# Kernel optimization log

Hardware: AMD Instinct MI355X
Metric: run time of the kernel (lower is better)

Reference implementation:

```python
import jax, jax.numpy as jnp
import numpy as np

TOP_K = 2

def setup_inputs() -> dict:
    key = jax.random.key(0)
    k1, k2 = jax.random.split(key)
    T, D, E = 16384, 2048, 64  # num_tokens, d_model, num_experts
    x = jax.random.normal(k1, (T, D), dtype=jnp.float32)
    Wg = jax.random.normal(k2, (D, E), dtype=jnp.float32) / np.sqrt(D)
    return {"x": x, "Wg": Wg}

def reference(x, Wg):
    T, E = x.shape[0], Wg.shape[1]
    # gate logits + softmax over experts
    logits = x @ Wg                                   # [T, E]
    probs = jax.nn.softmax(logits, axis=-1)           # [T, E]
    # top-k expert selection, renormalize selected weights
    top_vals, top_idx = jax.lax.top_k(probs, TOP_K)   # [T, K]
    top_vals = top_vals / jnp.sum(top_vals, axis=-1, keepdims=True)
    # scatter sparse gate weights into dense [T, E]
    rows = jnp.arange(T)[:, None]                     # [T, 1]
    gate_weights = jnp.zeros_like(probs).at[rows, top_idx].set(top_vals)
    # load-balance aux loss: E * sum_e f_e * P_e
    mask = jnp.sum(jax.nn.one_hot(top_idx, E, dtype=probs.dtype), axis=1)  # [T, E]
    f = jnp.mean(mask, axis=0)    # fraction of tokens routed to each expert
    P = jnp.mean(probs, axis=0)   # mean router prob per expert
    aux_loss = E * jnp.sum(f * P)
    return gate_weights, top_idx, aux_loss
```

## Files before the change

### kernel.cpp

```cpp
#include <hip/hip_runtime.h>


typedef __attribute__((ext_vector_type(8))) _Float16 half8;
typedef __attribute__((ext_vector_type(4))) float f32x4;

constexpr int DD  = 2048;
constexpr int EE  = 64;
constexpr int BM  = 16;
constexpr int BK  = 64;
constexpr int NCH = DD / BK;

#define WVM(N) asm volatile("s_waitcnt vmcnt(" #N ")" ::: "memory")
#define BAR()  asm volatile("s_barrier" ::: "memory")

__global__ __launch_bounds__(256) void wsplit_kernel(
    const float* __restrict__ Wg, _Float16* __restrict__ wF)
{
    __shared__ float xl[32][65];
    const int tid = threadIdx.x;
    const int kc  = blockIdx.x;
    const int k0  = kc * 32;
#pragma unroll
    for (int r = 0; r < 2; ++r) {
        int slot = tid + r * 256;
        int row = slot >> 4, c4 = (slot & 15) << 2;
        *(float4*)&xl[row][c4] = *(const float4*)&Wg[(size_t)(k0 + row) * EE + c4];
    }
    __syncthreads();
    const int t = tid >> 6, l = tid & 63;
    const int e  = t * 16 + (l & 15);
    const int kl = (l >> 4) * 8;
    half8 hh, ll;
#pragma unroll
    for (int j = 0; j < 8; ++j) {
        float v = xl[kl + j][e];
        _Float16 h = (_Float16)v;
        hh[j] = h;
        ll[j] = (_Float16)((v - (float)h) * 4096.f);
    }
    const size_t base = ((size_t)(kc * 4 + t) * 2) * 512 + (size_t)l * 8;
    *(half8*)&wF[base]       = hh;
    *(half8*)&wF[base + 512] = ll;
}

__global__ __launch_bounds__(256, 4) void gate_kernel(
    const float* __restrict__ x, const _Float16* __restrict__ wF,
    float* __restrict__ gate_out, float* __restrict__ idx_out,
    float* __restrict__ pSum, float* __restrict__ pCnt)
{
    __shared__ __align__(16) float xs[4][BM][BK];
    __shared__ float red[2][BM][68];
    __shared__ float auxsm[2][4][64];

    const int tid  = threadIdx.x;
    const int wv   = tid >> 6;
    const int lane = tid & 63;
    const int kh   = wv & 1;
    const int nh   = wv >> 1;
    const size_t tok0 = (size_t)blockIdx.x * BM;
    const float* xg = x + tok0 * DD;

    const int srow = tid >> 4;
    const int scb  = (tid & 15) << 4;
    const int ssb  = scb ^ ((srow & 7) << 5);
    auto stageX = [&](int buf, int c) {
        __builtin_amdgcn_global_load_lds(
            xg + (size_t)srow * DD + c * BK + (ssb >> 2),
            &xs[buf][srow][scb >> 2], 16, 0, 0);
    };

    const size_t tile0 = (((size_t)kh * 4 + nh * 2) * 2) * 512 + (size_t)lane * 8;
    const _Float16* w00 = wF + tile0;
    const _Float16* w01 = wF + tile0 + 512;
    const _Float16* w10 = wF + tile0 + 1024;
    const _Float16* w11 = wF + tile0 + 1536;
    half8 wA0, wA1, wA2, wA3, wB0, wB1, wB2, wB3;

#define LOADW(R0, R1, R2, R3, c)                                               \
    do { const size_t o = (size_t)(c) * 8192;                                  \
         R0 = *(const half8*)(w00 + o); R1 = *(const half8*)(w01 + o);         \
         R2 = *(const half8*)(w10 + o); R3 = *(const half8*)(w11 + o); } while (0)

    f32x4 aH0 = {0.f,0.f,0.f,0.f}, aL0 = {0.f,0.f,0.f,0.f};
    f32x4 aH1 = {0.f,0.f,0.f,0.f}, aL1 = {0.f,0.f,0.f,0.f};

    const int rrow = lane & 15;
    const int rfb  = (kh * 128 + (lane >> 4) * 32) ^ ((rrow & 7) << 5);

#define COMPUTE(buf, W0, W1, W2, W3)                                           \
    do {                                                                       \
        const float* p = (const float*)((const char*)&xs[buf][rrow][0] + rfb); \
        float4 xa = *(const float4*)p;                                         \
        float4 xb = *(const float4*)(p + 4);                                   \
        half8 ah, al; float v;                                                 \
        v = xa.x; { _Float16 h=(_Float16)v; ah[0]=h; al[0]=(_Float16)((v-(float)h)*4096.f); } \
        v = xa.y; { _Float16 h=(_Float16)v; ah[1]=h; al[1]=(_Float16)((v-(float)h)*4096.f); } \
        v = xa.z; { _Float16 h=(_Float16)v; ah[2]=h; al[2]=(_Float16)((v-(float)h)*4096.f); } \
        v = xa.w; { _Float16 h=(_Float16)v; ah[3]=h; al[3]=(_Float16)((v-(float)h)*4096.f); } \
        v = xb.x; { _Float16 h=(_Float16)v; ah[4]=h; al[4]=(_Float16)((v-(float)h)*4096.f); } \
        v = xb.y; { _Float16 h=(_Float16)v; ah[5]=h; al[5]=(_Float16)((v-(float)h)*4096.f); } \
        v = xb.z; { _Float16 h=(_Float16)v; ah[6]=h; al[6]=(_Float16)((v-(float)h)*4096.f); } \
        v = xb.w; { _Float16 h=(_Float16)v; ah[7]=h; al[7]=(_Float16)((v-(float)h)*4096.f); } \
        aH0 = __builtin_amdgcn_mfma_f32_16x16x32_f16(ah, W0, aH0, 0, 0, 0);    \
        aL0 = __builtin_amdgcn_mfma_f32_16x16x32_f16(ah, W1, aL0, 0, 0, 0);    \
        aL0 = __builtin_amdgcn_mfma_f32_16x16x32_f16(al, W0, aL0, 0, 0, 0);    \
        aH1 = __builtin_amdgcn_mfma_f32_16x16x32_f16(ah, W2, aH1, 0, 0, 0);    \
        aL1 = __builtin_amdgcn_mfma_f32_16x16x32_f16(ah, W3, aL1, 0, 0, 0);    \
        aL1 = __builtin_amdgcn_mfma_f32_16x16x32_f16(al, W2, aL1, 0, 0, 0);    \
    } while (0)

    stageX(0, 0);
    stageX(1, 1);
    LOADW(wA0, wA1, wA2, wA3, 0);
    stageX(2, 2);
    LOADW(wB0, wB1, wB2, wB3, 1);

#pragma unroll 1
    for (int c = 0; c < NCH; ++c) {
        if (c < NCH - 1) { WVM(5); } else { WVM(0); }
        BAR();
        if (c & 1) {
            COMPUTE(c & 3, wB0, wB1, wB2, wB3);
            if (c + 2 < NCH) LOADW(wB0, wB1, wB2, wB3, c + 2);
        } else {
            COMPUTE(c & 3, wA0, wA1, wA2, wA3);
            if (c + 2 < NCH) LOADW(wA0, wA1, wA2, wA3, c + 2);
        }
        if (c + 3 < NCH) stageX((c + 3) & 3, c + 3);
        BAR();
    }
#undef LOADW
#undef COMPUTE

    const float inv = 1.f / 4096.f;
#pragma unroll
    for (int e = 0; e < 4; ++e) {
        const int row = (lane >> 4) * 4 + e;
        red[kh][row][nh * 32 + (lane & 15)]      = aH0[e] + aL0[e] * inv;
        red[kh][row][nh * 32 + 16 + (lane & 15)] = aH1[e] + aL1[e] * inv;
    }
    __syncthreads();

    float sumP_acc = 0.f;
    float cnt_acc  = 0.f;
#pragma unroll 1
    for (int tt = 0; tt < 4; ++tt) {
        const int tl = wv * 4 + tt;
        const size_t t = tok0 + tl;
        float v = red[0][tl][lane] + red[1][tl][lane];

        float m = v;
#pragma unroll
        for (int off = 32; off; off >>= 1) m = fmaxf(m, __shfl_xor(m, off, 64));
        float p = expf(v - m);
        float s = p;
#pragma unroll
        for (int off = 32; off; off >>= 1) s += __shfl_xor(s, off, 64);
        float prob = p / s;
        sumP_acc += prob;

        float bv = prob; int bi = lane;
#pragma unroll
        for (int off = 32; off; off >>= 1) {
            float ov = __shfl_xor(bv, off, 64);
            int   oi = __shfl_xor(bi, off, 64);
            if (ov > bv || (ov == bv && oi < bi)) { bv = ov; bi = oi; }
        }
        float v2 = (lane == bi) ? -1.f : prob;
        float bv2 = v2; int bi2 = lane;
#pragma unroll
        for (int off = 32; off; off >>= 1) {
            float ov = __shfl_xor(bv2, off, 64);
            int   oi = __shfl_xor(bi2, off, 64);
            if (ov > bv2 || (ov == bv2 && oi < bi2)) { bv2 = ov; bi2 = oi; }
        }

        float denom = bv + bv2;
        float g1 = bv / denom, g2 = bv2 / denom;
        float g = (lane == bi) ? g1 : ((lane == bi2) ? g2 : 0.f);
        gate_out[t * EE + lane] = g;
        if (lane == 0) {
            idx_out[2 * t]     = (float)bi;
            idx_out[2 * t + 1] = (float)bi2;
        }
        cnt_acc += (lane == bi)  ? 1.f : 0.f;
        cnt_acc += (lane == bi2) ? 1.f : 0.f;
    }

    auxsm[0][wv][lane] = sumP_acc;
    auxsm[1][wv][lane] = cnt_acc;
    __syncthreads();
    if (wv == 0) {
        float sp = 0.f, c2 = 0.f;
#pragma unroll
        for (int w = 0; w < 4; ++w) {
            sp += auxsm[0][w][lane];
            c2 += auxsm[1][w][lane];
        }
        pSum[(size_t)blockIdx.x * 64 + lane] = sp;
        pCnt[(size_t)blockIdx.x * 64 + lane] = c2;
    }
}

__global__ __launch_bounds__(1024) void aux_kernel(
    const float* __restrict__ pSum, const float* __restrict__ pCnt,
    float* __restrict__ aux_out, int nblocks, float scale)
{
    const int tid  = threadIdx.x;
    const int wv   = tid >> 6;
    const int lane = tid & 63;
    __shared__ float smem[2][16][64];

    float sp[4] = {0.f, 0.f, 0.f, 0.f};
    float cc[4] = {0.f, 0.f, 0.f, 0.f};
    for (int b = wv * 4; b < nblocks; b += 64) {
#pragma unroll
        for (int u = 0; u < 4; ++u) {
            sp[u] += pSum[(size_t)(b + u) * 64 + lane];
            cc[u] += pCnt[(size_t)(b + u) * 64 + lane];
        }
    }
    smem[0][wv][lane] = (sp[0] + sp[1]) + (sp[2] + sp[3]);
    smem[1][wv][lane] = (cc[0] + cc[1]) + (cc[2] + cc[3]);
    __syncthreads();
    if (wv == 0) {
        float SP = 0.f, C = 0.f;
#pragma unroll
        for (int w = 0; w < 16; ++w) {
            SP += smem[0][w][lane];
            C  += smem[1][w][lane];
        }
        float prod = SP * C;
#pragma unroll
        for (int off = 32; off; off >>= 1) prod += __shfl_xor(prod, off, 64);
        if (lane == 0) aux_out[0] = prod * scale;
    }
}

extern "C" void kernel_launch(void* const* d_in, const int* in_sizes, int n_in,
                              void* d_out, int out_size, void* d_ws, size_t ws_size,
                              hipStream_t stream) {
    const float* x  = (const float*)d_in[0];
    const float* Wg = (const float*)d_in[1];
    const int T = in_sizes[0] / DD;

    float* out      = (float*)d_out;
    float* gate_out = out;
    float* idx_out  = out + (size_t)T * EE;
    float* aux_out  = idx_out + (size_t)T * 2;

    const int nblocks = T / BM;
    _Float16* wF = (_Float16*)d_ws;
    float* pSum = (float*)(wF + (size_t)64 * 4 * 2 * 512);
    float* pCnt = pSum + (size_t)nblocks * 64;

    wsplit_kernel<<<64, 256, 0, stream>>>(Wg, wF);
    gate_kernel<<<nblocks, 256, 0, stream>>>(x, wF, gate_out, idx_out, pSum, pCnt);

    const float scale = (float)EE / ((float)T * (float)T);
    aux_kernel<<<1, 1024, 0, stream>>>(pSum, pCnt, aux_out, nblocks, scale);
}
```

Before: 56.55 us.

## Split K across four waves with full expert width and wider K chunks

Each of the four waves now owns a quarter of a 128-wide K chunk and computes all 64 experts, instead of a 2x2 split over K and experts. The K chunk doubles, the x staging ring drops from four buffers to three, and the epilogue buffers share LDS with the staging buffers through a union. Weight fragments are loaded inside compute instead of being register double-buffered. The aim is fewer loop iterations and barriers with more MFMA work per wave, but weight-load latency is now exposed within each step and there is one less buffer of prefetch depth.

Measured after the change: 53.89 us. 4.7% less time.

```diff
diff --git a/kernel.cpp b/kernel.cpp
--- a/kernel.cpp
+++ b/kernel.cpp
@@ -7,7 +7,7 @@
 constexpr int DD  = 2048;
 constexpr int EE  = 64;
 constexpr int BM  = 16;
-constexpr int BK  = 64;
+constexpr int BK  = 128;
 constexpr int NCH = DD / BK;
 
 #define WVM(N) asm volatile("s_waitcnt vmcnt(" #N ")" ::: "memory")
@@ -38,7 +38,7 @@
         hh[j] = h;
         ll[j] = (_Float16)((v - (float)h) * 4096.f);
     }
-    const size_t base = ((size_t)(kc * 4 + t) * 2) * 512 + (size_t)l * 8;
+    const size_t base = (size_t)(kc * 8 + t * 2) * 512 + (size_t)l * 8;
     *(half8*)&wF[base]       = hh;
     *(half8*)&wF[base + 512] = ll;
 }
@@ -48,96 +48,91 @@
     float* __restrict__ gate_out, float* __restrict__ idx_out,
     float* __restrict__ pSum, float* __restrict__ pCnt)
 {
-    __shared__ __align__(16) float xs[4][BM][BK];
-    __shared__ float red[2][BM][68];
-    __shared__ float auxsm[2][4][64];
+    __shared__ __align__(16) union {
+        float xs[3][BM][BK];
+        struct { float red[4][BM][68]; float auxsm[2][4][64]; } ep;
+    } sm;
 
     const int tid  = threadIdx.x;
-    const int wv   = tid >> 6;
+    const int kq   = tid >> 6;
     const int lane = tid & 63;
-    const int kh   = wv & 1;
-    const int nh   = wv >> 1;
     const size_t tok0 = (size_t)blockIdx.x * BM;
     const float* xg = x + tok0 * DD;
 
-    const int srow = tid >> 4;
-    const int scb  = (tid & 15) << 4;
-    const int ssb  = scb ^ ((srow & 7) << 5);
     auto stageX = [&](int buf, int c) {
-        __builtin_amdgcn_global_load_lds(
-            xg + (size_t)srow * DD + c * BK + (ssb >> 2),
-            &xs[buf][srow][scb >> 2], 16, 0, 0);
+#pragma unroll
+        for (int r = 0; r < 2; ++r) {
+            int slot = tid + r * 256;
+            int row  = slot >> 5;
+            int cb   = (slot & 31) << 4;
+            int sb   = cb ^ ((row & 7) << 5);
+            __builtin_amdgcn_global_load_lds(
+                xg + (size_t)row * DD + c * BK + (sb >> 2),
+                &sm.xs[buf][row][cb >> 2], 16, 0, 0);
+        }
     };
 
-    const size_t tile0 = (((size_t)kh * 4 + nh * 2) * 2) * 512 + (size_t)lane * 8;
-    const _Float16* w00 = wF + tile0;
-    const _Float16* w01 = wF + tile0 + 512;
-    const _Float16* w10 = wF + tile0 + 1024;
-    const _Float16* w11 = wF + tile0 + 1536;
-    half8 wA0, wA1, wA2, wA3, wB0, wB1, wB2, wB3;
-
-#define LOADW(R0, R1, R2, R3, c)                                               \
-    do { const size_t o = (size_t)(c) * 8192;                                  \
-         R0 = *(const half8*)(w00 + o); R1 = *(const half8*)(w01 + o);         \
-         R2 = *(const half8*)(w10 + o); R3 = *(const half8*)(w11 + o); } while (0)
-
-    f32x4 aH0 = {0.f,0.f,0.f,0.f}, aL0 = {0.f,0.f,0.f,0.f};
-    f32x4 aH1 = {0.f,0.f,0.f,0.f}, aL1 = {0.f,0.f,0.f,0.f};
+    f32x4 aH[4], aL[4];
+#pragma unroll
+    for (int t = 0; t < 4; ++t) {
+        aH[t] = (f32x4){0.f, 0.f, 0.f, 0.f};
+        aL[t] = (f32x4){0.f, 0.f, 0.f, 0.f};
+    }
 
     const int rrow = lane & 15;
-    const int rfb  = (kh * 128 + (lane >> 4) * 32) ^ ((rrow & 7) << 5);
-
-#define COMPUTE(buf, W0, W1, W2, W3)                                           \
-    do {                                                                       \
-        const float* p = (const float*)((const char*)&xs[buf][rrow][0] + rfb); \
-        float4 xa = *(const float4*)p;                                         \
-        float4 xb = *(const float4*)(p + 4);                                   \
-        half8 ah, al; float v;                                                 \
-        v = xa.x; { _Float16 h=(_Float16)v; ah[0]=h; al[0]=(_Float16)((v-(float)h)*4096.f); } \
-        v = xa.y; { _Float16 h=(_Float16)v; ah[1]=h; al[1]=(_Float16)((v-(float)h)*4096.f); } \
-        v = xa.z; { _Float16 h=(_Float16)v; ah[2]=h; al[2]=(_Float16)((v-(float)h)*4096.f); } \
-        v = xa.w; { _Float16 h=(_Float16)v; ah[3]=h; al[3]=(_Float16)((v-(float)h)*4096.f); } \
-        v = xb.x; { _Float16 h=(_Float16)v; ah[4]=h; al[4]=(_Float16)((v-(float)h)*4096.f); } \
-        v = xb.y; { _Float16 h=(_Float16)v; ah[5]=h; al[5]=(_Float16)((v-(float)h)*4096.f); } \
-        v = xb.z; { _Float16 h=(_Float16)v; ah[6]=h; al[6]=(_Float16)((v-(float)h)*4096.f); } \
-        v = xb.w; { _Float16 h=(_Float16)v; ah[7]=h; al[7]=(_Float16)((v-(float)h)*4096.f); } \
-        aH0 = __builtin_amdgcn_mfma_f32_16x16x32_f16(ah, W0, aH0, 0, 0, 0);    \
-        aL0 = __builtin_amdgcn_mfma_f32_16x16x32_f16(ah, W1, aL0, 0, 0, 0);    \
-        aL0 = __builtin_amdgcn_mfma_f32_16x16x32_f16(al, W0, aL0, 0, 0, 0);    \
-        aH1 = __builtin_amdgcn_mfma_f32_16x16x32_f16(ah, W2, aH1, 0, 0, 0);    \
-        aL1 = __builtin_amdgcn_mfma_f32_16x16x32_f16(ah, W3, aL1, 0, 0, 0);    \
-        aL1 = __builtin_amdgcn_mfma_f32_16x16x32_f16(al, W2, aL1, 0, 0, 0);    \
-    } while (0)
+    const int rb   = (kq * 128 + ((lane >> 4) * 32)) ^ ((rrow & 7) << 5);
+
+    auto compute = [&](int buf, int c) {
+        const _Float16* wb = wF + (size_t)(c * 4 + kq) * 4096 + (size_t)lane * 8;
+        half8 wh[4], wl[4];
+#pragma unroll
+        for (int t = 0; t < 4; ++t) {
+            wh[t] = *(const half8*)(wb + (t * 2) * 512);
+            wl[t] = *(const half8*)(wb + (t * 2 + 1) * 512);
+        }
+        const float* p = (const float*)((const char*)&sm.xs[buf][rrow][0] + rb);
+        float4 xa = *(const float4*)p;
+        float4 xb = *(const float4*)(p + 4);
+        half8 ah, al;
+        {
+            float v;
+            v = xa.x; { _Float16 h=(_Float16)v; ah[0]=h; al[0]=(_Float16)((v-(float)h)*4096.f); }
+            v = xa.y; { _Float16 h=(_Float16)v; ah[1]=h; al[1]=(_Float16)((v-(float)h)*4096.f); }
+            v = xa.z; { _Float16 h=(_Float16)v; ah[2]=h; al[2]=(_Float16)((v-(float)h)*4096.f); }
+            v = xa.w; { _Float16 h=(_Float16)v; ah[3]=h; al[3]=(_Float16)((v-(float)h)*4096.f); }
+            v = xb.x; { _Float16 h=(_Float16)v; ah[4]=h; al[4]=(_Float16)((v-(float)h)*4096.f); }
+            v = xb.y; { _Float16 h=(_Float16)v; ah[5]=h; al[5]=(_Float16)((v-(float)h)*4096.f); }
+            v = xb.z; { _Float16 h=(_Float16)v; ah[6]=h; al[6]=(_Float16)((v-(float)h)*4096.f); }
+            v = xb.w; { _Float16 h=(_Float16)v; ah[7]=h; al[7]=(_Float16)((v-(float)h)*4096.f); }
+        }
+#pragma unroll
+        for (int t = 0; t < 4; ++t) {
+            aH[t] = __builtin_amdgcn_mfma_f32_16x16x32_f16(ah, wh[t], aH[t], 0, 0, 0);
+            aL[t] = __builtin_amdgcn_mfma_f32_16x16x32_f16(ah, wl[t], aL[t], 0, 0, 0);
+            aL[t] = __builtin_amdgcn_mfma_f32_16x16x32_f16(al, wh[t], aL[t], 0, 0, 0);
+        }
+    };
 
     stageX(0, 0);
     stageX(1, 1);
-    LOADW(wA0, wA1, wA2, wA3, 0);
-    stageX(2, 2);
-    LOADW(wB0, wB1, wB2, wB3, 1);
 
 #pragma unroll 1
     for (int c = 0; c < NCH; ++c) {
-        if (c < NCH - 1) { WVM(5); } else { WVM(0); }
+        if (c < NCH - 1) { WVM(2); } else { WVM(0); }
         BAR();
-        if (c & 1) {
-            COMPUTE(c & 3, wB0, wB1, wB2, wB3);
-            if (c + 2 < NCH) LOADW(wB0, wB1, wB2, wB3, c + 2);
-        } else {
-            COMPUTE(c & 3, wA0, wA1, wA2, wA3);
-            if (c + 2 < NCH) LOADW(wA0, wA1, wA2, wA3, c + 2);
-        }
-        if (c + 3 < NCH) stageX((c + 3) & 3, c + 3);
+        compute(c % 3, c);
         BAR();
-    }
-#undef LOADW
-#undef COMPUTE
-
+        if (c + 2 < NCH) stageX((c + 2) % 3, c + 2);
+    }
+
+    __syncthreads();
     const float inv = 1.f / 4096.f;
 #pragma unroll
     for (int e = 0; e < 4; ++e) {
         const int row = (lane >> 4) * 4 + e;
-        red[kh][row][nh * 32 + (lane & 15)]      = aH0[e] + aL0[e] * inv;
-        red[kh][row][nh * 32 + 16 + (lane & 15)] = aH1[e] + aL1[e] * inv;
+#pragma unroll
+        for (int t = 0; t < 4; ++t)
+            sm.ep.red[kq][row][t * 16 + (lane & 15)] = aH[t][e] + aL[t][e] * inv;
     }
     __syncthreads();
 
@@ -145,9 +140,10 @@
     float cnt_acc  = 0.f;
 #pragma unroll 1
     for (int tt = 0; tt < 4; ++tt) {
-        const int tl = wv * 4 + tt;
+        const int tl = kq * 4 + tt;
         const size_t t = tok0 + tl;
-        float v = red[0][tl][lane] + red[1][tl][lane];
+        float v = (sm.ep.red[0][tl][lane] + sm.ep.red[1][tl][lane])
+                + (sm.ep.red[2][tl][lane] + sm.ep.red[3][tl][lane]);
 
         float m = v;
 #pragma unroll
@@ -187,15 +183,15 @@
         cnt_acc += (lane == bi2) ? 1.f : 0.f;
     }
 
-    auxsm[0][wv][lane] = sumP_acc;
-    auxsm[1][wv][lane] = cnt_acc;
-    __syncthreads();
-    if (wv == 0) {
+    sm.ep.auxsm[0][kq][lane] = sumP_acc;
+    sm.ep.auxsm[1][kq][lane] = cnt_acc;
+    __syncthreads();
+    if (kq == 0) {
         float sp = 0.f, c2 = 0.f;
 #pragma unroll
         for (int w = 0; w < 4; ++w) {
-            sp += auxsm[0][w][lane];
-            c2 += auxsm[1][w][lane];
+            sp += sm.ep.auxsm[0][w][lane];
+            c2 += sm.ep.auxsm[1][w][lane];
         }
         pSum[(size_t)blockIdx.x * 64 + lane] = sp;
         pCnt[(size_t)blockIdx.x * 64 + lane] = c2;
@@ -251,7 +247,7 @@
 
     const int nblocks = T / BM;
     _Float16* wF = (_Float16*)d_ws;
-    float* pSum = (float*)(wF + (size_t)64 * 4 * 2 * 512);
+    float* pSum = (float*)(wF + (size_t)64 * 8 * 512);
     float* pCnt = pSum + (size_t)nblocks * 64;
 
     wsplit_kernel<<<64, 256, 0, stream>>>(Wg, wF);
```
